# Optimization experiments

Measured on AMD Instinct MI355X. Metric: run time of the kernel, lower is better.

Reference implementation:

```python
import jax, jax.numpy as jnp
import numpy as np


def _dF(field, c):
    """Central differences of component c of field [B,X,Y,Z,C] -> [B,X-2,Y-2,Z-2,3]."""
    f = field[..., c]
    dx = (f[:, 2:, 1:-1, 1:-1] - f[:, :-2, 1:-1, 1:-1]) * 0.5
    dy = (f[:, 1:-1, 2:, 1:-1] - f[:, 1:-1, :-2, 1:-1]) * 0.5
    dz = (f[:, 1:-1, 1:-1, 2:] - f[:, 1:-1, 1:-1, :-2]) * 0.5
    return jnp.stack((dx, dy, dz), axis=4)


def setup_inputs() -> dict:
    key = jax.random.key(0)
    grid = jax.random.normal(key, (2, 160, 160, 160, 3), dtype=jnp.float32)
    return {"grid": grid}


def reference(grid):
    # First derivatives of each displacement component: [B,X-2,Y-2,Z-2,3]
    dx = _dF(grid, 0)
    dy = _dF(grid, 1)
    dz = _dF(grid, 2)
    # Second derivatives: [B,X-4,Y-4,Z-4,3]
    dxx = _dF(dx, 0)
    dyy = _dF(dy, 1)
    dzz = _dF(dz, 2)
    dxy = _dF(dx, 1)
    dyz = _dF(dy, 2)
    dxz = _dF(dx, 2)
    penalty = jnp.sum(dxx ** 2 + dyy ** 2 + dzz ** 2
                      + 2.0 * (dxy ** 2 + dyz ** 2 + dxz ** 2))
    return penalty / dxx.size
```

## Files before the change

kernel.cpp:

```cpp
#include <hip/hip_runtime.h>

#define OY 480
#define OX 76800
#define SB 12288000
#define RST 60
#define SLC 960
#define IT 12
#define NSEG 13
#define NBLK 3380
#define INV_SIZE (1.0f/22778496.0f)

#define ROW_SHL1 0x101
#define ROW_SHL2 0x102
#define ROW_SHR1 0x111
#define ROW_SHR2 0x112

template<int CTRL>
__device__ __forceinline__ float dppf(float x){
    return __int_as_float(__builtin_amdgcn_update_dpp(
        0, __float_as_int(x), CTRL, 0xF, 0xF, true));
}

__device__ __forceinline__ float4 ld4p(const float* p){ return *reinterpret_cast<const float4*>(p); }
__device__ __forceinline__ void st4p(float* p, float4 v){ *reinterpret_cast<float4*>(p) = v; }

#define STEPX(S, V0a, V0b, DP, SBc, SBn) { \
    if ((S) <= 13) { \
        const float* bp = Gs + (size_t)((S)+2)*OX; \
        SBn[0]=ld4p(bp+gof0); SBn[1]=ld4p(bp+gof1); SBn[2]=ld4p(bp+gof2); \
        if (wv3) SBn[3]=ld4p(bp+gof3); \
    } \
    if (qact) { \
        const float* Lr = lds + ((S)%3)*SLC + oj; \
        float x[24]; \
        { float4 y0=ld4p(Lr),y1=ld4p(Lr+4),y2=ld4p(Lr+8),y3=ld4p(Lr+12),y4=ld4p(Lr+16),y5=ld4p(Lr+20); \
          x[0]=y0.x;x[1]=y0.y;x[2]=y0.z;x[3]=y0.w; x[4]=y1.x;x[5]=y1.y;x[6]=y1.z;x[7]=y1.w; \
          x[8]=y2.x;x[9]=y2.y;x[10]=y2.z;x[11]=y2.w; x[12]=y3.x;x[13]=y3.y;x[14]=y3.z;x[15]=y3.w; \
          x[16]=y4.x;x[17]=y4.y;x[18]=y4.z;x[19]=y4.w; x[20]=y5.x;x[21]=y5.y;x[22]=y5.z;x[23]=y5.w; } \
        float dz0[4],dz1[4],dz2[4],dy0[4],dy1[4],v0c[4]; \
        _Pragma("unroll") for (int v=0; v<4; ++v) { \
            v0c[v] = x[3*v+6]; \
            dz0[v] = x[3*v+9]-x[3*v+3]; dz1[v]=x[3*v+10]-x[3*v+4]; dz2[v]=x[3*v+11]-x[3*v+5]; \
            dy0[v] = dppf<ROW_SHR1>(x[3*v+6]) - dppf<ROW_SHL1>(x[3*v+6]); \
            dy1[v] = dppf<ROW_SHR1>(x[3*v+7]) - dppf<ROW_SHL1>(x[3*v+7]); \
        } \
        if ((S) >= 2 && (S) <= 13) { \
            _Pragma("unroll") for (int v=0; v<4; ++v) { \
                float c0=x[3*v+6], c1=x[3*v+7]; \
                float hy0 = dppf<ROW_SHR2>(c0) - 2.f*c0 + dppf<ROW_SHL2>(c0); \
                float hy1 = dppf<ROW_SHR2>(c1) - 2.f*c1 + dppf<ROW_SHL2>(c1); \
                float yz0 = dppf<ROW_SHR1>(dz0[v]) - dppf<ROW_SHL1>(dz0[v]); \
                float yz1 = dppf<ROW_SHR1>(dz1[v]) - dppf<ROW_SHL1>(dz1[v]); \
                float yz2 = dppf<ROW_SHR1>(dz2[v]) - dppf<ROW_SHL1>(dz2[v]); \
                if (vr) { \
                    float zz0 = x[3*v+12]-2.f*x[3*v+6]+x[3*v]; \
                    float zz1 = x[3*v+13]-2.f*x[3*v+7]+x[3*v+1]; \
                    float zz2 = x[3*v+14]-2.f*x[3*v+8]+x[3*v+2]; \
                    cls2=fmaf(zz0,zz0,cls2); cls2=fmaf(zz1,zz1,cls2); cls1=fmaf(zz2,zz2,cls1); \
                    cls2=fmaf(hy0,hy0,cls2); cls1=fmaf(hy1,hy1,cls1); \
                    cls4=fmaf(yz0,yz0,cls4); cls3=fmaf(yz1,yz1,cls3); cls1=fmaf(yz2,yz2,cls1); \
                } \
            } \
        } \
        _Pragma("unroll") for (int v=0; v<4; ++v) { \
            if (vr && (S) >= 3 && (S) <= 14) { float h; \
                h=dy0[v]-DP[0][v]; cls3=fmaf(h,h,cls3); \
                h=dy1[v]-DP[1][v]; cls1=fmaf(h,h,cls1); \
                h=dz0[v]-DP[2][v]; cls3=fmaf(h,h,cls3); \
                h=dz1[v]-DP[3][v]; cls2=fmaf(h,h,cls2); \
                h=dz2[v]-DP[4][v]; cls1=fmaf(h,h,cls1); \
            } \
            DP[0][v]=dy0[v]; DP[1][v]=dy1[v]; DP[2][v]=dz0[v]; DP[3][v]=dz1[v]; DP[4][v]=dz2[v]; \
            if (vr && (S) >= 4) { float h = v0c[v]-2.f*V0a[v]+V0b[v]; cls1=fmaf(h,h,cls1); } \
            V0b[v]=V0a[v]; V0a[v]=v0c[v]; \
        } \
    } \
    if ((S) <= 14) { \
        float* Lw = lds + (((S)+1)%3)*SLC; \
        st4p(Lw+lof0, SBc[0]); st4p(Lw+lof1, SBc[1]); st4p(Lw+lof2, SBc[2]); \
        if (wv3) st4p(Lw+lof3, SBc[3]); \
    } \
}

__global__ __launch_bounds__(64)
void be_partials(const float* __restrict__ g, float* __restrict__ partial) {
    __shared__ float lds[3*SLC];

    const int tid = threadIdx.x;
    const int bid = blockIdx.x;
    const int is = bid % NSEG;
    int r1 = bid / NSEG;
    const int zt = r1 % 10; r1 /= 10;
    const int jt = r1 % 13;
    const int bb = r1 / 13;

    const int j0 = 2 + jt*12;
    const int wb = (zt < 9) ? 48*zt : 420;
    const int i0 = 2 + is*IT;
    const float* __restrict__ Gs =
        g + (size_t)bb*SB + (size_t)(j0-2)*OY + wb + (size_t)(i0-2)*OX;

    int gof0,gof1,gof2,gof3,lof0,lof1,lof2,lof3;
    { int f,row,pos;
      f=tid;     row=f/15; pos=f-15*row; gof0=row*OY+4*pos; lof0=row*RST+4*pos;
      f=tid+64;  row=f/15; pos=f-15*row; gof1=row*OY+4*pos; lof1=row*RST+4*pos;
      f=tid+128; row=f/15; pos=f-15*row; gof2=row*OY+4*pos; lof2=row*RST+4*pos;
      f=tid+192; row=f/15; pos=f-15*row; gof3=row*OY+4*pos; lof3=row*RST+4*pos; }
    const bool wv3 = tid < 48;
    if (!wv3) { gof3 = gof0; lof3 = lof0; }

    const int r = tid & 15;
    const int Q = tid >> 4;
    const int qmax = (zt == 9) ? 3 : 4;
    const bool qact = Q < qmax;
    const bool vr = (r >= 2) && (r <= 13);
    const int oj = r*RST + 12*Q + ((zt == 9) ? 12 : 0);

    float4 sA[4], sB[4];
    float v0A0[4],v0A1[4],v0B0[4],v0B1[4];
    float dpA[5][4], dpB[5][4];
    #pragma unroll
    for (int v=0; v<4; ++v) {
        v0A0[v]=v0A1[v]=v0B0[v]=v0B1[v]=0.f;
        #pragma unroll
        for (int q=0; q<5; ++q) { dpA[q][v]=0.f; dpB[q][v]=0.f; }
    }
    float cls1=0.f, cls2=0.f, cls3=0.f, cls4=0.f;

    { float4 a0=ld4p(Gs+gof0), a1=ld4p(Gs+gof1), a2=ld4p(Gs+gof2);
      st4p(lds+lof0,a0); st4p(lds+lof1,a1); st4p(lds+lof2,a2);
      if (wv3) { float4 a3=ld4p(Gs+gof3); st4p(lds+lof3,a3); } }
    { const float* bp = Gs + OX;
      sB[0]=ld4p(bp+gof0); sB[1]=ld4p(bp+gof1); sB[2]=ld4p(bp+gof2);
      if (wv3) sB[3]=ld4p(bp+gof3); }

    STEPX( 0, v0A0,v0A1,dpA, sB, sA)
    STEPX( 1, v0B0,v0B1,dpB, sA, sB)
    STEPX( 2, v0A0,v0A1,dpA, sB, sA)
    STEPX( 3, v0B0,v0B1,dpB, sA, sB)
    STEPX( 4, v0A0,v0A1,dpA, sB, sA)
    STEPX( 5, v0B0,v0B1,dpB, sA, sB)
    STEPX( 6, v0A0,v0A1,dpA, sB, sA)
    STEPX( 7, v0B0,v0B1,dpB, sA, sB)
    STEPX( 8, v0A0,v0A1,dpA, sB, sA)
    STEPX( 9, v0B0,v0B1,dpB, sA, sB)
    STEPX(10, v0A0,v0A1,dpA, sB, sA)
    STEPX(11, v0B0,v0B1,dpB, sA, sB)
    STEPX(12, v0A0,v0A1,dpA, sB, sA)
    STEPX(13, v0B0,v0B1,dpB, sA, sB)
    STEPX(14, v0A0,v0A1,dpA, sB, sA)
    STEPX(15, v0B0,v0B1,dpB, sA, sB)

    float sv = fmaf(2.f, cls2, cls1);
    sv = fmaf(3.f, cls3, sv);
    sv = fmaf(4.f, cls4, sv);
    sv *= 0.0625f;

    #pragma unroll
    for (int off = 32; off > 0; off >>= 1) sv += __shfl_down(sv, off, 64);
    if (tid == 0) partial[bid] = sv;
}

__global__ __launch_bounds__(256)
void be_final(const float* __restrict__ partial, float* __restrict__ out) {
    float s = 0.0f;
    for (int i = threadIdx.x; i < NBLK; i += 256) s += partial[i];
    #pragma unroll
    for (int off = 32; off > 0; off >>= 1) s += __shfl_down(s, off, 64);
    __shared__ float ws[4];
    if ((threadIdx.x & 63) == 0) ws[threadIdx.x >> 6] = s;
    __syncthreads();
    if (threadIdx.x == 0)
        out[0] = ((ws[0] + ws[1]) + (ws[2] + ws[3])) * INV_SIZE;
}

extern "C" void kernel_launch(void* const* d_in, const int* in_sizes, int n_in,
                              void* d_out, int out_size, void* d_ws, size_t ws_size,
                              hipStream_t stream) {
    const float* grid = (const float*)d_in[0];
    float* out = (float*)d_out;
    float* partials = (float*)d_ws;

    be_partials<<<dim3(NBLK), dim3(64), 0, stream>>>(grid, partials);
    be_final<<<1, 256, 0, stream>>>(partials, out);
}
```

Measured before the change: 156.1 us.

## Process two z-tiles per block with interleaved steps in a runtime loop

Each block now handles two z-tiles (A and B) with separate LDS ring buffers and register states, halving the block count and interleaving their steps so one tile's global loads overlap the other's compute. The fully unrolled 16-step sequence becomes a runtime loop over 8 double-steps, so the step-index conditions are evaluated at runtime rather than folded at compile time. This doubles LDS and register state per block, which risks lower occupancy and extra branching.

```diff
diff --git a/kernel.cpp b/kernel.cpp
--- a/kernel.cpp
+++ b/kernel.cpp
@@ -7,7 +7,7 @@
 #define SLC 960
 #define IT 12
 #define NSEG 13
-#define NBLK 3380
+#define NBLK 1690
 #define INV_SIZE (1.0f/22778496.0f)
 
 #define ROW_SHL1 0x101
@@ -24,14 +24,14 @@
 __device__ __forceinline__ float4 ld4p(const float* p){ return *reinterpret_cast<const float4*>(p); }
 __device__ __forceinline__ void st4p(float* p, float4 v){ *reinterpret_cast<float4*>(p) = v; }
 
-#define STEPX(S, V0a, V0b, DP, SBc, SBn) { \
-    if ((S) <= 13) { \
-        const float* bp = Gs + (size_t)((S)+2)*OX; \
+#define STEPT(s, V0a, V0b, DP, SBc, SBn, GT, LT, ojT, qactT) { \
+    if ((s) <= 13) { \
+        const float* bp = GT + (size_t)((s)+2)*OX; \
         SBn[0]=ld4p(bp+gof0); SBn[1]=ld4p(bp+gof1); SBn[2]=ld4p(bp+gof2); \
         if (wv3) SBn[3]=ld4p(bp+gof3); \
     } \
-    if (qact) { \
-        const float* Lr = lds + ((S)%3)*SLC + oj; \
+    if (qactT) { \
+        const float* Lr = LT + ((s)%3)*SLC + ojT; \
         float x[24]; \
         { float4 y0=ld4p(Lr),y1=ld4p(Lr+4),y2=ld4p(Lr+8),y3=ld4p(Lr+12),y4=ld4p(Lr+16),y5=ld4p(Lr+20); \
           x[0]=y0.x;x[1]=y0.y;x[2]=y0.z;x[3]=y0.w; x[4]=y1.x;x[5]=y1.y;x[6]=y1.z;x[7]=y1.w; \
@@ -44,7 +44,7 @@
             dy0[v] = dppf<ROW_SHR1>(x[3*v+6]) - dppf<ROW_SHL1>(x[3*v+6]); \
             dy1[v] = dppf<ROW_SHR1>(x[3*v+7]) - dppf<ROW_SHL1>(x[3*v+7]); \
         } \
-        if ((S) >= 2 && (S) <= 13) { \
+        if ((s) >= 2 && (s) <= 13) { \
             _Pragma("unroll") for (int v=0; v<4; ++v) { \
                 float c0=x[3*v+6], c1=x[3*v+7]; \
                 float hy0 = dppf<ROW_SHR2>(c0) - 2.f*c0 + dppf<ROW_SHL2>(c0); \
@@ -63,7 +63,7 @@
             } \
         } \
         _Pragma("unroll") for (int v=0; v<4; ++v) { \
-            if (vr && (S) >= 3 && (S) <= 14) { float h; \
+            if (vr && (s) >= 3 && (s) <= 14) { float h; \
                 h=dy0[v]-DP[0][v]; cls3=fmaf(h,h,cls3); \
                 h=dy1[v]-DP[1][v]; cls1=fmaf(h,h,cls1); \
                 h=dz0[v]-DP[2][v]; cls3=fmaf(h,h,cls3); \
@@ -71,12 +71,12 @@
                 h=dz2[v]-DP[4][v]; cls1=fmaf(h,h,cls1); \
             } \
             DP[0][v]=dy0[v]; DP[1][v]=dy1[v]; DP[2][v]=dz0[v]; DP[3][v]=dz1[v]; DP[4][v]=dz2[v]; \
-            if (vr && (S) >= 4) { float h = v0c[v]-2.f*V0a[v]+V0b[v]; cls1=fmaf(h,h,cls1); } \
+            if (vr && (s) >= 4) { float h = v0c[v]-2.f*V0a[v]+V0b[v]; cls1=fmaf(h,h,cls1); } \
             V0b[v]=V0a[v]; V0a[v]=v0c[v]; \
         } \
     } \
-    if ((S) <= 14) { \
-        float* Lw = lds + (((S)+1)%3)*SLC; \
+    if ((s) <= 14) { \
+        float* Lw = LT + (((s)+1)%3)*SLC; \
         st4p(Lw+lof0, SBc[0]); st4p(Lw+lof1, SBc[1]); st4p(Lw+lof2, SBc[2]); \
         if (wv3) st4p(Lw+lof3, SBc[3]); \
     } \
@@ -84,21 +84,28 @@
 
 __global__ __launch_bounds__(64)
 void be_partials(const float* __restrict__ g, float* __restrict__ partial) {
-    __shared__ float lds[3*SLC];
+    __shared__ float lds[6*SLC];
 
     const int tid = threadIdx.x;
     const int bid = blockIdx.x;
     const int is = bid % NSEG;
     int r1 = bid / NSEG;
-    const int zt = r1 % 10; r1 /= 10;
+    const int ztp = r1 % 5; r1 /= 5;
     const int jt = r1 % 13;
     const int bb = r1 / 13;
 
+    const int ztA = ztp;
+    const int ztB = ztp + 5;
     const int j0 = 2 + jt*12;
-    const int wb = (zt < 9) ? 48*zt : 420;
     const int i0 = 2 + is*IT;
-    const float* __restrict__ Gs =
-        g + (size_t)bb*SB + (size_t)(j0-2)*OY + wb + (size_t)(i0-2)*OX;
+    const int wbA = 48*ztA;
+    const int wbB = (ztB < 9) ? 48*ztB : 420;
+    const float* __restrict__ GA =
+        g + (size_t)bb*SB + (size_t)(j0-2)*OY + wbA + (size_t)(i0-2)*OX;
+    const float* __restrict__ GB =
+        g + (size_t)bb*SB + (size_t)(j0-2)*OY + wbB + (size_t)(i0-2)*OX;
+    float* __restrict__ ldsA = lds;
+    float* __restrict__ ldsB = lds + 3*SLC;
 
     int gof0,gof1,gof2,gof3,lof0,lof1,lof2,lof3;
     { int f,row,pos;
@@ -111,45 +118,46 @@
 
     const int r = tid & 15;
     const int Q = tid >> 4;
-    const int qmax = (zt == 9) ? 3 : 4;
-    const bool qact = Q < qmax;
+    const bool qactB = (ztB == 9) ? (Q < 3) : true;
     const bool vr = (r >= 2) && (r <= 13);
-    const int oj = r*RST + 12*Q + ((zt == 9) ? 12 : 0);
+    const int ojA = r*RST + 12*Q;
+    const int ojB = r*RST + 12*Q + ((ztB == 9) ? 12 : 0);
 
-    float4 sA[4], sB[4];
-    float v0A0[4],v0A1[4],v0B0[4],v0B1[4];
-    float dpA[5][4], dpB[5][4];
+    float4 sA0[4], sA1[4], sB0[4], sB1[4];
+    float vAe0[4],vAe1[4],vAo0[4],vAo1[4], vBe0[4],vBe1[4],vBo0[4],vBo1[4];
+    float dpAe[5][4], dpAo[5][4], dpBe[5][4], dpBo[5][4];
     #pragma unroll
     for (int v=0; v<4; ++v) {
-        v0A0[v]=v0A1[v]=v0B0[v]=v0B1[v]=0.f;
+        vAe0[v]=vAe1[v]=vAo0[v]=vAo1[v]=0.f;
+        vBe0[v]=vBe1[v]=vBo0[v]=vBo1[v]=0.f;
         #pragma unroll
-        for (int q=0; q<5; ++q) { dpA[q][v]=0.f; dpB[q][v]=0.f; }
+        for (int q=0; q<5; ++q) {
+            dpAe[q][v]=dpAo[q][v]=0.f; dpBe[q][v]=dpBo[q][v]=0.f;
+        }
     }
     float cls1=0.f, cls2=0.f, cls3=0.f, cls4=0.f;
 
-    { float4 a0=ld4p(Gs+gof0), a1=ld4p(Gs+gof1), a2=ld4p(Gs+gof2);
-      st4p(lds+lof0,a0); st4p(lds+lof1,a1); st4p(lds+lof2,a2);
-      if (wv3) { float4 a3=ld4p(Gs+gof3); st4p(lds+lof3,a3); } }
-    { const float* bp = Gs + OX;
-      sB[0]=ld4p(bp+gof0); sB[1]=ld4p(bp+gof1); sB[2]=ld4p(bp+gof2);
-      if (wv3) sB[3]=ld4p(bp+gof3); }
+    { float4 a0=ld4p(GA+gof0), a1=ld4p(GA+gof1), a2=ld4p(GA+gof2);
+      st4p(ldsA+lof0,a0); st4p(ldsA+lof1,a1); st4p(ldsA+lof2,a2);
+      if (wv3) { float4 a3=ld4p(GA+gof3); st4p(ldsA+lof3,a3); } }
+    { float4 a0=ld4p(GB+gof0), a1=ld4p(GB+gof1), a2=ld4p(GB+gof2);
+      st4p(ldsB+lof0,a0); st4p(ldsB+lof1,a1); st4p(ldsB+lof2,a2);
+      if (wv3) { float4 a3=ld4p(GB+gof3); st4p(ldsB+lof3,a3); } }
+    { const float* bp = GA + OX;
+      sA1[0]=ld4p(bp+gof0); sA1[1]=ld4p(bp+gof1); sA1[2]=ld4p(bp+gof2);
+      if (wv3) sA1[3]=ld4p(bp+gof3); }
+    { const float* bp = GB + OX;
+      sB1[0]=ld4p(bp+gof0); sB1[1]=ld4p(bp+gof1); sB1[2]=ld4p(bp+gof2);
+      if (wv3) sB1[3]=ld4p(bp+gof3); }
 
-    STEPX( 0, v0A0,v0A1,dpA, sB, sA)
-    STEPX( 1, v0B0,v0B1,dpB, sA, sB)
-    STEPX( 2, v0A0,v0A1,dpA, sB, sA)
-    STEPX( 3, v0B0,v0B1,dpB, sA, sB)
-    STEPX( 4, v0A0,v0A1,dpA, sB, sA)
-    STEPX( 5, v0B0,v0B1,dpB, sA, sB)
-    STEPX( 6, v0A0,v0A1,dpA, sB, sA)
-    STEPX( 7, v0B0,v0B1,dpB, sA, sB)
-    STEPX( 8, v0A0,v0A1,dpA, sB, sA)
-    STEPX( 9, v0B0,v0B1,dpB, sA, sB)
-    STEPX(10, v0A0,v0A1,dpA, sB, sA)
-    STEPX(11, v0B0,v0B1,dpB, sA, sB)
-    STEPX(12, v0A0,v0A1,dpA, sB, sA)
-    STEPX(13, v0B0,v0B1,dpB, sA, sB)
-    STEPX(14, v0A0,v0A1,dpA, sB, sA)
-    STEPX(15, v0B0,v0B1,dpB, sA, sB)
+    #pragma unroll 1
+    for (int d = 0; d < 8; ++d) {
+        const int s0 = 2*d, s1 = 2*d + 1;
+        STEPT(s0, vAe0,vAe1,dpAe, sA1,sA0, GA, ldsA, ojA, true)
+        STEPT(s0, vBe0,vBe1,dpBe, sB1,sB0, GB, ldsB, ojB, qactB)
+        STEPT(s1, vAo0,vAo1,dpAo, sA0,sA1, GA, ldsA, ojA, true)
+        STEPT(s1, vBo0,vBo1,dpBo, sB0,sB1, GB, ldsB, ojB, qactB)
+    }
 
     float sv = fmaf(2.f, cls2, cls1);
     sv = fmaf(3.f, cls3, sv);
```

Result: slower. 168.6 us (+8.0%).

## Stage input slices directly into LDS with async global_load_lds ring buffer

Applied to the files above, without the earlier changes.

Replaces the register-staged global load followed by an LDS store with `__builtin_amdgcn_global_load_lds` (16-byte), which writes each slice straight into shared memory. The LDS buffer grows from a 3-slot to a 5-slot ring and prefetches three slices ahead, gated by explicit `s_waitcnt vmcnt` counts. The aim is to drop the float4 staging registers and the ds_write traffic, and to hide more load latency. In exchange it uses more LDS per block and depends on hand-tuned vmcnt values, which must match the number of loads in flight.

```diff
diff --git a/kernel.cpp b/kernel.cpp
--- a/kernel.cpp
+++ b/kernel.cpp
@@ -4,7 +4,7 @@
 #define OX 76800
 #define SB 12288000
 #define RST 60
-#define SLC 960
+#define SLC 1024
 #define IT 12
 #define NSEG 13
 #define NBLK 3380
@@ -22,16 +22,28 @@
 }
 
 __device__ __forceinline__ float4 ld4p(const float* p){ return *reinterpret_cast<const float4*>(p); }
-__device__ __forceinline__ void st4p(float* p, float4 v){ *reinterpret_cast<float4*>(p) = v; }
 
-#define STEPX(S, V0a, V0b, DP, SBc, SBn) { \
-    if ((S) <= 13) { \
-        const float* bp = Gs + (size_t)((S)+2)*OX; \
-        SBn[0]=ld4p(bp+gof0); SBn[1]=ld4p(bp+gof1); SBn[2]=ld4p(bp+gof2); \
-        if (wv3) SBn[3]=ld4p(bp+gof3); \
+__device__ __forceinline__ void stage16(const float* gp, float* lp){
+    __builtin_amdgcn_global_load_lds(
+        (const __attribute__((address_space(1))) void*)gp,
+        (__attribute__((address_space(3))) void*)lp,
+        16, 0, 0);
+}
+
+#define WAITVM(n) asm volatile("s_waitcnt vmcnt(" #n ")" ::: "memory")
+
+#define STEPX(S, N, V0a, V0b, DP) { \
+    if ((S)+3 <= 15) { \
+        const float* bp = Gs + (size_t)((S)+3)*OX; \
+        float* Ld = lds + (((S)+3)%5)*SLC; \
+        stage16(bp+goff0, Ld); \
+        stage16(bp+goff1, Ld+256); \
+        stage16(bp+goff2, Ld+512); \
+        stage16(bp+goff3, Ld+768); \
     } \
+    WAITVM(N); \
     if (qact) { \
-        const float* Lr = lds + ((S)%3)*SLC + oj; \
+        const float* Lr = lds + ((S)%5)*SLC + oj; \
         float x[24]; \
         { float4 y0=ld4p(Lr),y1=ld4p(Lr+4),y2=ld4p(Lr+8),y3=ld4p(Lr+12),y4=ld4p(Lr+16),y5=ld4p(Lr+20); \
           x[0]=y0.x;x[1]=y0.y;x[2]=y0.z;x[3]=y0.w; x[4]=y1.x;x[5]=y1.y;x[6]=y1.z;x[7]=y1.w; \
@@ -75,16 +87,11 @@
             V0b[v]=V0a[v]; V0a[v]=v0c[v]; \
         } \
     } \
-    if ((S) <= 14) { \
-        float* Lw = lds + (((S)+1)%3)*SLC; \
-        st4p(Lw+lof0, SBc[0]); st4p(Lw+lof1, SBc[1]); st4p(Lw+lof2, SBc[2]); \
-        if (wv3) st4p(Lw+lof3, SBc[3]); \
-    } \
 }
 
 __global__ __launch_bounds__(64)
 void be_partials(const float* __restrict__ g, float* __restrict__ partial) {
-    __shared__ float lds[3*SLC];
+    __shared__ float lds[5*SLC];
 
     const int tid = threadIdx.x;
     const int bid = blockIdx.x;
@@ -100,14 +107,12 @@
     const float* __restrict__ Gs =
         g + (size_t)bb*SB + (size_t)(j0-2)*OY + wb + (size_t)(i0-2)*OX;
 
-    int gof0,gof1,gof2,gof3,lof0,lof1,lof2,lof3;
-    { int f,row,pos;
-      f=tid;     row=f/15; pos=f-15*row; gof0=row*OY+4*pos; lof0=row*RST+4*pos;
-      f=tid+64;  row=f/15; pos=f-15*row; gof1=row*OY+4*pos; lof1=row*RST+4*pos;
-      f=tid+128; row=f/15; pos=f-15*row; gof2=row*OY+4*pos; lof2=row*RST+4*pos;
-      f=tid+192; row=f/15; pos=f-15*row; gof3=row*OY+4*pos; lof3=row*RST+4*pos; }
-    const bool wv3 = tid < 48;
-    if (!wv3) { gof3 = gof0; lof3 = lof0; }
+    int goff0, goff1, goff2, goff3;
+    { int f, vp;
+      f = tid;       vp = f;                 goff0 = (vp/15)*OY + 4*(vp%15);
+      f = tid + 64;  vp = f;                 goff1 = (vp/15)*OY + 4*(vp%15);
+      f = tid + 128; vp = f;                 goff2 = (vp/15)*OY + 4*(vp%15);
+      f = tid + 192; vp = (f < 240) ? f : 239; goff3 = (vp/15)*OY + 4*(vp%15); }
 
     const int r = tid & 15;
     const int Q = tid >> 4;
@@ -116,7 +121,6 @@
     const bool vr = (r >= 2) && (r <= 13);
     const int oj = r*RST + 12*Q + ((zt == 9) ? 12 : 0);
 
-    float4 sA[4], sB[4];
     float v0A0[4],v0A1[4],v0B0[4],v0B1[4];
     float dpA[5][4], dpB[5][4];
     #pragma unroll
@@ -127,29 +131,32 @@
     }
     float cls1=0.f, cls2=0.f, cls3=0.f, cls4=0.f;
 
-    { float4 a0=ld4p(Gs+gof0), a1=ld4p(Gs+gof1), a2=ld4p(Gs+gof2);
-      st4p(lds+lof0,a0); st4p(lds+lof1,a1); st4p(lds+lof2,a2);
-      if (wv3) { float4 a3=ld4p(Gs+gof3); st4p(lds+lof3,a3); } }
-    { const float* bp = Gs + OX;
-      sB[0]=ld4p(bp+gof0); sB[1]=ld4p(bp+gof1); sB[2]=ld4p(bp+gof2);
-      if (wv3) sB[3]=ld4p(bp+gof3); }
+    #pragma unroll
+    for (int sl = 0; sl < 3; ++sl) {
+        const float* bp = Gs + (size_t)sl*OX;
+        float* Ld = lds + sl*SLC;
+        stage16(bp+goff0, Ld);
+        stage16(bp+goff1, Ld+256);
+        stage16(bp+goff2, Ld+512);
+        stage16(bp+goff3, Ld+768);
+    }
 
-    STEPX( 0, v0A0,v0A1,dpA, sB, sA)
-    STEPX( 1, v0B0,v0B1,dpB, sA, sB)
-    STEPX( 2, v0A0,v0A1,dpA, sB, sA)
-    STEPX( 3, v0B0,v0B1,dpB, sA, sB)
-    STEPX( 4, v0A0,v0A1,dpA, sB, sA)
-    STEPX( 5, v0B0,v0B1,dpB, sA, sB)
-    STEPX( 6, v0A0,v0A1,dpA, sB, sA)
-    STEPX( 7, v0B0,v0B1,dpB, sA, sB)
-    STEPX( 8, v0A0,v0A1,dpA, sB, sA)
-    STEPX( 9, v0B0,v0B1,dpB, sA, sB)
-    STEPX(10, v0A0,v0A1,dpA, sB, sA)
-    STEPX(11, v0B0,v0B1,dpB, sA, sB)
-    STEPX(12, v0A0,v0A1,dpA, sB, sA)
-    STEPX(13, v0B0,v0B1,dpB, sA, sB)
-    STEPX(14, v0A0,v0A1,dpA, sB, sA)
-    STEPX(15, v0B0,v0B1,dpB, sA, sB)
+    STEPX( 0, 12, v0A0,v0A1,dpA)
+    STEPX( 1, 12, v0B0,v0B1,dpB)
+    STEPX( 2, 12, v0A0,v0A1,dpA)
+    STEPX( 3, 12, v0B0,v0B1,dpB)
+    STEPX( 4, 12, v0A0,v0A1,dpA)
+    STEPX( 5, 12, v0B0,v0B1,dpB)
+    STEPX( 6, 12, v0A0,v0A1,dpA)
+    STEPX( 7, 12, v0B0,v0B1,dpB)
+    STEPX( 8, 12, v0A0,v0A1,dpA)
+    STEPX( 9, 12, v0B0,v0B1,dpB)
+    STEPX(10, 12, v0A0,v0A1,dpA)
+    STEPX(11, 12, v0B0,v0B1,dpB)
+    STEPX(12, 12, v0A0,v0A1,dpA)
+    STEPX(13,  8, v0B0,v0B1,dpB)
+    STEPX(14,  4, v0A0,v0A1,dpA)
+    STEPX(15,  0, v0B0,v0B1,dpB)
 
     float sv = fmaf(2.f, cls2, cls1);
     sv = fmaf(3.f, cls3, sv);
```

After: 160.8 us. +3.0%, slower.
